# Performance work log

Hardware: AMD Instinct MI355X
Metric: run time of the kernel (lower is better)

The kernel has to match this reference:

```python
import jax, jax.numpy as jnp
import numpy as np

EPS = 1e-8
ANGULAR_WEIGHT = 0.1
L2_REG = 1e-4


def gram_schmidt_batch(A):
    # A: (B, 3, 3); orthogonalize the COLUMNS
    u1 = A[:, :, 0]
    e1 = u1 / (jnp.linalg.norm(u1, axis=1, keepdims=True) + EPS)
    a2 = A[:, :, 1]
    u2 = a2 - jnp.sum(e1 * a2, axis=1, keepdims=True) * e1
    e2 = u2 / (jnp.linalg.norm(u2, axis=1, keepdims=True) + EPS)
    a3 = A[:, :, 2]
    u3 = a3 - jnp.sum(e1 * a3, axis=1, keepdims=True) * e1 - jnp.sum(e2 * a3, axis=1, keepdims=True) * e2
    e3 = u3 / (jnp.linalg.norm(u3, axis=1, keepdims=True) + EPS)
    Q = jnp.stack([e1, e2, e3], axis=2)  # (B,3,3), columns e1,e2,e3
    det = jnp.linalg.det(Q)
    # flip third column where det < 0 to ensure proper rotation
    e3_fixed = jnp.where(det[:, None] < 0, -Q[:, :, 2], Q[:, :, 2])
    return Q.at[:, :, 2].set(e3_fixed)


def nine_d_to_rotmat(nine_d):
    A = jnp.clip(nine_d, -10.0, 10.0).reshape(-1, 3, 3)
    return gram_schmidt_batch(A)


def angular_distance(pred_9d, target_9d):
    pred_rot = nine_d_to_rotmat(pred_9d)
    target_rot = nine_d_to_rotmat(target_9d)
    # trace(pred^T @ target) = sum over all entries of elementwise product
    traces = jnp.einsum('bij,bij->b', pred_rot, target_rot)
    traces = jnp.clip(traces, -3.0 + 1e-6, 3.0 - 1e-6)
    cos_angle = jnp.clip((traces - 1.0) / 2.0, -1.0 + 1e-7, 1.0 - 1e-7)
    angles_deg = jnp.arccos(cos_angle) * (180.0 / np.pi)
    return jnp.where(jnp.isnan(angles_deg), 180.0, angles_deg)


def orthogonality_loss(nine_d):
    B = nine_d.shape[0]
    M = nine_d.reshape(B, 3, 3)
    AtA = jnp.einsum('bki,bkj->bij', M, M)
    diff = AtA - jnp.eye(3, dtype=nine_d.dtype)
    return jnp.mean(jnp.sum(diff * diff, axis=(1, 2)))


def setup_inputs() -> dict:
    key = jax.random.key(0)
    k1, k2 = jax.random.split(key)
    B = 4194304
    return {
        'pred_delta_9d': jax.random.normal(k1, (B, 9), dtype=jnp.float32),
        'target_delta_9d': jax.random.normal(k2, (B, 9), dtype=jnp.float32),
    }


def reference(pred_delta_9d, target_delta_9d):
    pred_delta_9d = jnp.clip(pred_delta_9d, -10.0, 10.0)
    pred_rot = nine_d_to_rotmat(pred_delta_9d)
    target_rot = nine_d_to_rotmat(target_delta_9d)
    diff = pred_rot - target_rot
    chordal_loss = jnp.mean(jnp.sum(diff * diff, axis=(1, 2)))
    angular_loss_term = jnp.mean(angular_distance(pred_delta_9d, target_delta_9d))
    ortho_loss = orthogonality_loss(pred_delta_9d)
    l2_loss = jnp.mean(pred_delta_9d ** 2)
    total_loss = chordal_loss + ANGULAR_WEIGHT * angular_loss_term + 0.01 * ortho_loss + L2_REG * l2_loss
    # NaN fallback: MSE between pred and target
    fallback = jnp.mean((pred_delta_9d - target_delta_9d) ** 2)
    return jnp.where(jnp.isnan(total_loss), fallback, total_loss)
```

## Files before the change

### kernel.cpp

```cpp
#include <hip/hip_runtime.h>
#include <math.h>

#define EPS_GS 1e-8f
#define RAD2DEG 57.29577951308232f
#define PI_F 3.14159265358979f

constexpr int THREADS   = 256;
constexpr int TILE_ROTS = 512;
constexpr int TILE_F    = TILE_ROTS * 9;
constexpr int TILE_F2   = TILE_F / 2;
constexpr int F2_PER_TH = TILE_F2 / THREADS;
constexpr int NSLOTS    = 16;
constexpr int MAX_BLKS  = 1024;

__device__ __forceinline__ float clip10(float x) {
    x = x < -10.f ? -10.f : x;
    x = x >  10.f ?  10.f : x;
    return x;
}

__device__ __forceinline__ float fsqrt(float x) { return __builtin_amdgcn_sqrtf(x); }
__device__ __forceinline__ float frcp(float x)  { return __builtin_amdgcn_rcpf(x); }

__device__ __forceinline__ float fast_acos(float x) {
    float ax = fabsf(x);
    float p = fmaf(ax, -0.0187293f, 0.0742610f);
    p = fmaf(ax, p, -0.2121144f);
    p = fmaf(ax, p, 1.5707288f);
    float pos = fsqrt(1.f - ax) * p;
    return x >= 0.f ? pos : PI_F - pos;
}

__device__ __forceinline__ void gs_rotmat(const float* v, float* R) {
    float c0x = v[0], c0y = v[3], c0z = v[6];
    float c1x = v[1], c1y = v[4], c1z = v[7];
    float c2x = v[2], c2y = v[5], c2z = v[8];

    float s1 = fmaf(c0x, c0x, fmaf(c0y, c0y, c0z*c0z));
    float inv1 = frcp(fsqrt(s1) + EPS_GS);
    float e1x = c0x*inv1, e1y = c0y*inv1, e1z = c0z*inv1;

    float d = fmaf(e1x, c1x, fmaf(e1y, c1y, e1z*c1z));
    float u2x = fmaf(-d, e1x, c1x), u2y = fmaf(-d, e1y, c1y), u2z = fmaf(-d, e1z, c1z);
    float s2 = fmaf(u2x, u2x, fmaf(u2y, u2y, u2z*u2z));
    float inv2 = frcp(fsqrt(s2) + EPS_GS);
    float e2x = u2x*inv2, e2y = u2y*inv2, e2z = u2z*inv2;

    float d1 = fmaf(e1x, c2x, fmaf(e1y, c2y, e1z*c2z));
    float d2 = fmaf(e2x, c2x, fmaf(e2y, c2y, e2z*c2z));
    float u3x = fmaf(-d1, e1x, fmaf(-d2, e2x, c2x));
    float u3y = fmaf(-d1, e1y, fmaf(-d2, e2y, c2y));
    float u3z = fmaf(-d1, e1z, fmaf(-d2, e2z, c2z));
    float s3 = fmaf(u3x, u3x, fmaf(u3y, u3y, u3z*u3z));
    float inv3 = frcp(fsqrt(s3) + EPS_GS);
    float e3x = u3x*inv3, e3y = u3y*inv3, e3z = u3z*inv3;

    float cxx = e2y*e3z - e2z*e3y;
    float cxy = e2z*e3x - e2x*e3z;
    float cxz = e2x*e3y - e2y*e3x;
    float det = fmaf(e1x, cxx, fmaf(e1y, cxy, e1z*cxz));
    if (det < 0.f) { e3x = -e3x; e3y = -e3y; e3z = -e3z; }

    R[0] = e1x; R[1] = e2x; R[2] = e3x;
    R[3] = e1y; R[4] = e2y; R[5] = e3y;
    R[6] = e1z; R[7] = e2z; R[8] = e3z;
}

__device__ __forceinline__ void accum_rot(const float* pr, const float* tg,
                                          float& lt, float& lf) {
    float pc[9], tc[9];
    #pragma unroll
    for (int m = 0; m < 9; ++m) { pc[m] = clip10(pr[m]); tc[m] = clip10(tg[m]); }

    float Rp[9], Rt[9];
    gs_rotmat(pc, Rp);
    gs_rotmat(tc, Rt);

    float chord = 0.f, tr = 0.f;
    #pragma unroll
    for (int m = 0; m < 9; ++m) {
        float d = Rp[m] - Rt[m];
        chord = fmaf(d, d, chord);
        tr    = fmaf(Rp[m], Rt[m], tr);
    }

    const float trLo = -3.0f + 1e-6f, trHi = 3.0f - 1e-6f;
    tr = tr < trLo ? trLo : (tr > trHi ? trHi : tr);
    float ca = (tr - 1.f) * 0.5f;
    const float cLo = -1.0f + 1e-7f, cHi = 1.0f - 1e-7f;
    ca = ca < cLo ? cLo : (ca > cHi ? cHi : ca);
    float ang = fast_acos(ca) * RAD2DEG;
    if (ang != ang) ang = 180.f;

    float o = 0.f;
    #pragma unroll
    for (int i = 0; i < 3; ++i) {
        float dii = fmaf(pc[i], pc[i], fmaf(pc[3+i], pc[3+i], pc[6+i]*pc[6+i])) - 1.f;
        o = fmaf(dii, dii, o);
    }
    #pragma unroll
    for (int i = 0; i < 3; ++i) {
        #pragma unroll
        for (int j = i + 1; j < 3; ++j) {
            float s = fmaf(pc[i], pc[j], fmaf(pc[3+i], pc[3+j], pc[6+i]*pc[6+j]));
            float s2 = s + s;
            o = fmaf(s2, s, o);
        }
    }

    float l2 = 0.f, fb = 0.f;
    #pragma unroll
    for (int m = 0; m < 9; ++m) {
        l2 = fmaf(pc[m], pc[m], l2);
        float d = pc[m] - tg[m];
        fb = fmaf(d, d, fb);
    }

    lt += fmaf(0.1f, ang, chord) + fmaf(0.01f, o, (1e-4f/9.f)*l2);
    lf += fb;
}

__global__ __launch_bounds__(THREADS, 4)
void rot_loss_kernel(const float* __restrict__ pred, const float* __restrict__ targ,
                     double* __restrict__ acc, int B) {
    __shared__ float sp[TILE_F];
    __shared__ float sq[TILE_F];
    __shared__ float rsum_t[4], rsum_f[4];

    const int tid    = threadIdx.x;
    const int ntiles = (B + TILE_ROTS - 1) / TILE_ROTS;

    float lt = 0.f, lf = 0.f;

    float2 pv[F2_PER_TH], tv[F2_PER_TH];

    auto issue_loads = [&](int t) {
        const float2* p2 = reinterpret_cast<const float2*>(pred) + (size_t)t * TILE_F2;
        const float2* q2 = reinterpret_cast<const float2*>(targ) + (size_t)t * TILE_F2;
        #pragma unroll
        for (int k = 0; k < F2_PER_TH; ++k) pv[k] = p2[tid + k*THREADS];
        #pragma unroll
        for (int k = 0; k < F2_PER_TH; ++k) tv[k] = q2[tid + k*THREADS];
    };
    auto tile_full = [&](int t) {
        return (size_t)(t + 1) * TILE_ROTS <= (size_t)B;
    };

    int t0 = blockIdx.x;
    if (t0 < ntiles && tile_full(t0)) issue_loads(t0);

    for (int t = t0; t < ntiles; t += gridDim.x) {
        const size_t rot0 = (size_t)t * TILE_ROTS;
        if (tile_full(t)) {
            float2* sp2 = reinterpret_cast<float2*>(sp);
            float2* sq2 = reinterpret_cast<float2*>(sq);
            #pragma unroll
            for (int k = 0; k < F2_PER_TH; ++k) {
                sp2[tid + k*THREADS] = pv[k];
                sq2[tid + k*THREADS] = tv[k];
            }
            __syncthreads();
            const int tn = t + gridDim.x;
            if (tn < ntiles && tile_full(tn)) issue_loads(tn);
            #pragma unroll
            for (int rr = 0; rr < 2; ++rr) {
                const int r = tid + rr*THREADS;
                accum_rot(&sp[9*r], &sq[9*r], lt, lf);
            }
            __syncthreads();
        } else {
            const int rem = (int)((size_t)B - rot0);
            for (int r = tid; r < rem; r += THREADS) {
                float a1[9], b1[9];
                const float* pp = pred + (rot0 + r) * 9;
                const float* qq = targ + (rot0 + r) * 9;
                for (int m = 0; m < 9; ++m) { a1[m] = pp[m]; b1[m] = qq[m]; }
                accum_rot(a1, b1, lt, lf);
            }
        }
    }

    #pragma unroll
    for (int off = 32; off > 0; off >>= 1) {
        lt += __shfl_down(lt, off, 64);
        lf += __shfl_down(lf, off, 64);
    }
    const int lane = tid & 63;
    const int wid  = tid >> 6;
    if (lane == 0) { rsum_t[wid] = lt; rsum_f[wid] = lf; }
    __syncthreads();
    if (tid == 0) {
        float bt = rsum_t[0] + rsum_t[1] + rsum_t[2] + rsum_t[3];
        float bf = rsum_f[0] + rsum_f[1] + rsum_f[2] + rsum_f[3];
        double* slot = acc + (size_t)(blockIdx.x & (NSLOTS - 1)) * 8;
        unsafeAtomicAdd(&slot[0], (double)bt);
        unsafeAtomicAdd(&slot[1], (double)bf);
    }
}

__global__ void finalize_kernel(const double* __restrict__ acc,
                                float* __restrict__ out, int B) {
    if (threadIdx.x == 0 && blockIdx.x == 0) {
        double t = 0.0, f = 0.0;
        for (int s = 0; s < NSLOTS; ++s) { t += acc[s*8]; f += acc[s*8 + 1]; }
        double total = t / (double)B;
        double fb    = f / (9.0 * (double)B);
        out[0] = isnan(total) ? (float)fb : (float)total;
    }
}

extern "C" void kernel_launch(void* const* d_in, const int* in_sizes, int n_in,
                              void* d_out, int out_size, void* d_ws, size_t ws_size,
                              hipStream_t stream) {
    const float* pred = (const float*)d_in[0];
    const float* targ = (const float*)d_in[1];
    const int n = in_sizes[0];
    const int B = n / 9;

    double* acc = (double*)d_ws;
    hipMemsetAsync(d_ws, 0, NSLOTS * 8 * sizeof(double), stream);

    const int ntiles = (B + TILE_ROTS - 1) / TILE_ROTS;
    const int blocks = ntiles < MAX_BLKS ? ntiles : MAX_BLKS;
    rot_loss_kernel<<<blocks, THREADS, 0, stream>>>(pred, targ, acc, B);
    finalize_kernel<<<1, 64, 0, stream>>>(acc, (float*)d_out, B);
}
```

Baseline: 378.9 us.

## Stage tiles via direct global-to-LDS loads with double buffering

Replaces the register-staged float2 loads and LDS stores with async global_load_lds 16-byte transfers into a double-buffered shared tile. The next tile is prefetched while the current one is computed, synchronised with a manual vmcnt wait and raw barriers. Grid size and the occupancy hint are halved to fit the doubled LDS footprint. This is meant to remove register pressure and the VGPR-to-LDS copy, but the hand-written vmcnt count is fragile and occupancy drops.

```diff
diff --git a/kernel.cpp b/kernel.cpp
--- a/kernel.cpp
+++ b/kernel.cpp
@@ -8,10 +8,12 @@
 constexpr int THREADS   = 256;
 constexpr int TILE_ROTS = 512;
 constexpr int TILE_F    = TILE_ROTS * 9;
-constexpr int TILE_F2   = TILE_F / 2;
-constexpr int F2_PER_TH = TILE_F2 / THREADS;
+constexpr int TILE_TOT  = TILE_F * 2;
+constexpr int CHUNK_F   = 256;
+constexpr int CHUNKS    = TILE_TOT / CHUNK_F;
+constexpr int CH_PER_W  = CHUNKS / 4;
 constexpr int NSLOTS    = 16;
-constexpr int MAX_BLKS  = 1024;
+constexpr int MAX_BLKS  = 512;
 
 __device__ __forceinline__ float clip10(float x) {
     x = x < -10.f ? -10.f : x;
@@ -21,6 +23,13 @@
 
 __device__ __forceinline__ float fsqrt(float x) { return __builtin_amdgcn_sqrtf(x); }
 __device__ __forceinline__ float frcp(float x)  { return __builtin_amdgcn_rcpf(x); }
+
+__device__ __forceinline__ void gload_lds16(const float* g, float* l) {
+    __builtin_amdgcn_global_load_lds(
+        (const __attribute__((address_space(1))) void*)g,
+        (__attribute__((address_space(3))) void*)l,
+        16, 0, 0);
+}
 
 __device__ __forceinline__ float fast_acos(float x) {
     float ax = fabsf(x);
@@ -120,55 +129,61 @@
     lf += fb;
 }
 
-__global__ __launch_bounds__(THREADS, 4)
+__global__ __launch_bounds__(THREADS, 2)
 void rot_loss_kernel(const float* __restrict__ pred, const float* __restrict__ targ,
                      double* __restrict__ acc, int B) {
-    __shared__ float sp[TILE_F];
-    __shared__ float sq[TILE_F];
+    __shared__ float buf[2][TILE_TOT];
     __shared__ float rsum_t[4], rsum_f[4];
 
     const int tid    = threadIdx.x;
+    const int wv     = tid >> 6;
+    const int lane   = tid & 63;
     const int ntiles = (B + TILE_ROTS - 1) / TILE_ROTS;
+    const int tstep  = gridDim.x;
 
     float lt = 0.f, lf = 0.f;
 
-    float2 pv[F2_PER_TH], tv[F2_PER_TH];
-
-    auto issue_loads = [&](int t) {
-        const float2* p2 = reinterpret_cast<const float2*>(pred) + (size_t)t * TILE_F2;
-        const float2* q2 = reinterpret_cast<const float2*>(targ) + (size_t)t * TILE_F2;
-        #pragma unroll
-        for (int k = 0; k < F2_PER_TH; ++k) pv[k] = p2[tid + k*THREADS];
-        #pragma unroll
-        for (int k = 0; k < F2_PER_TH; ++k) tv[k] = q2[tid + k*THREADS];
-    };
     auto tile_full = [&](int t) {
         return (size_t)(t + 1) * TILE_ROTS <= (size_t)B;
     };
-
-    int t0 = blockIdx.x;
-    if (t0 < ntiles && tile_full(t0)) issue_loads(t0);
-
-    for (int t = t0; t < ntiles; t += gridDim.x) {
-        const size_t rot0 = (size_t)t * TILE_ROTS;
+    auto stage = [&](int b, int t) {
+        const float* psrc = pred + (size_t)t * TILE_F;
+        const float* qsrc = targ + (size_t)t * TILE_F;
+        #pragma unroll
+        for (int k = 0; k < CH_PER_W; ++k) {
+            const int c = wv + 4*k;
+            const float* src = (c < 18) ? (psrc + (size_t)c * CHUNK_F)
+                                        : (qsrc + (size_t)(c - 18) * CHUNK_F);
+            gload_lds16(src + lane*4, &buf[b][c * CHUNK_F]);
+        }
+    };
+
+    const int t0 = blockIdx.x;
+    int cur = 0;
+    if (t0 < ntiles && tile_full(t0)) stage(0, t0);
+
+    for (int t = t0; t < ntiles; t += tstep) {
         if (tile_full(t)) {
-            float2* sp2 = reinterpret_cast<float2*>(sp);
-            float2* sq2 = reinterpret_cast<float2*>(sq);
-            #pragma unroll
-            for (int k = 0; k < F2_PER_TH; ++k) {
-                sp2[tid + k*THREADS] = pv[k];
-                sq2[tid + k*THREADS] = tv[k];
+            const int tn = t + tstep;
+            const bool nx = (tn < ntiles) && tile_full(tn);
+            if (nx) {
+                stage(cur ^ 1, tn);
+                asm volatile("s_waitcnt vmcnt(9)" ::: "memory");
+            } else {
+                asm volatile("s_waitcnt vmcnt(0)" ::: "memory");
             }
-            __syncthreads();
-            const int tn = t + gridDim.x;
-            if (tn < ntiles && tile_full(tn)) issue_loads(tn);
+            __builtin_amdgcn_s_barrier();
+            asm volatile("" ::: "memory");
             #pragma unroll
             for (int rr = 0; rr < 2; ++rr) {
                 const int r = tid + rr*THREADS;
-                accum_rot(&sp[9*r], &sq[9*r], lt, lf);
+                accum_rot(&buf[cur][9*r], &buf[cur][TILE_F + 9*r], lt, lf);
             }
-            __syncthreads();
+            asm volatile("" ::: "memory");
+            __builtin_amdgcn_s_barrier();
+            cur ^= 1;
         } else {
+            const size_t rot0 = (size_t)t * TILE_ROTS;
             const int rem = (int)((size_t)B - rot0);
             for (int r = tid; r < rem; r += THREADS) {
                 float a1[9], b1[9];
@@ -185,9 +200,7 @@
         lt += __shfl_down(lt, off, 64);
         lf += __shfl_down(lf, off, 64);
     }
-    const int lane = tid & 63;
-    const int wid  = tid >> 6;
-    if (lane == 0) { rsum_t[wid] = lt; rsum_f[wid] = lf; }
+    if (lane == 0) { rsum_t[wv] = lt; rsum_f[wv] = lf; }
     __syncthreads();
     if (tid == 0) {
         float bt = rsum_t[0] + rsum_t[1] + rsum_t[2] + rsum_t[3];
```

Result: faster. 316.9 us (-16.4%).
